# Kernel optimization log

Hardware: AMD Instinct MI355X
Metric: run time of the kernel (lower is better)

The kernel has to match this reference:

```python
import jax, jax.numpy as jnp
import numpy as np

V, H, B = 64, 128, 16384  # num_visible, num_hidden = alpha*V, batch of spin configs
ISCALE = 0.001


def setup_inputs() -> dict:
    key = jax.random.key(0)
    k1, k2, k3, k4 = jax.random.split(key, 4)
    x = jax.random.normal(k1, (B, V), dtype=jnp.float32)
    weight_1 = jax.random.normal(k2, (V, H), dtype=jnp.float32) * ISCALE
    weight_2 = jax.random.normal(k3, (H, V, V), dtype=jnp.float32) * (ISCALE / 10.0)
    hidden_bias = jax.random.normal(k4, (H,), dtype=jnp.float32) * ISCALE
    return {"x": x, "weight_1": weight_1, "weight_2": weight_2, "hidden_bias": hidden_bias}


def reference(x, weight_1, weight_2, hidden_bias):
    b, v = x.shape
    h = weight_2.shape[0]
    # order-1 term: (B,V) @ (V,H) -> (B,H)
    w1 = x @ weight_1
    # order-2 term: outer product of spins per sample, contracted with weight_2.
    # vis_ij: (B,V,V) flattened to (B,V*V); weight_2 flattened to (H,V*V) -> GEMM.
    vis_ij = jnp.einsum('mi,mj->mij', x, x).reshape(b, v * v)
    w2 = (vis_ij @ weight_2.reshape(h, v * v).T) * 0.5
    act = jnp.cos(hidden_bias + w1 + w2)  # (B,H)
    psi = jnp.prod(act, axis=-1)          # (B,)
    return psi
```

## Files before the change

kernel.cpp:

```cpp
#include <hip/hip_runtime.h>
#include <hip/hip_bf16.h>
#include <cstdint>

#define NV 64
#define NH 128
#define NB 16384
#define W2_ELEMS (NH * NV * NV)
#define W1_ELEMS (NV * NH)

typedef __bf16 bf16x8_t __attribute__((ext_vector_type(8)));
typedef float f32x4_t __attribute__((ext_vector_type(4)));
typedef uint32_t u32x4_t __attribute__((ext_vector_type(4)));

__device__ __forceinline__ uint32_t bf16_rne(float f) {
  uint32_t u = __float_as_uint(f);
  return (u + 0x7fffu + ((u >> 16) & 1u)) >> 16;
}

__global__ void cvt_kernel(const float* __restrict__ w1f,
                           const float* __restrict__ w2f,
                           uint16_t* __restrict__ wsW2,
                           uint16_t* __restrict__ wsW1) {
  int base = (blockIdx.x * 256 + threadIdx.x) * 4;
  const float* src;
  uint16_t* dst;
  int off;
  if (base < W2_ELEMS) { src = w2f; dst = wsW2; off = base; }
  else                 { src = w1f; dst = wsW1; off = base - W2_ELEMS; }
  float4 v = *(const float4*)(src + off);
  uint2 p;
  p.x = (bf16_rne(v.y) << 16) | bf16_rne(v.x);
  p.y = (bf16_rne(v.w) << 16) | bf16_rne(v.z);
  *(uint2*)(dst + off) = p;
}

__launch_bounds__(512, 2)
__global__ void rbm_kernel(const float* __restrict__ xg,
                           const float* __restrict__ biasg,
                           const __hip_bfloat16* __restrict__ w1g,
                           const __hip_bfloat16* __restrict__ w2g,
                           float* __restrict__ outg) {
  __shared__ __align__(16) __hip_bfloat16 btile[2][NH * 32];
  __shared__ __align__(16) __hip_bfloat16 xtile[64 * 72];
  __shared__ __align__(16) __hip_bfloat16 w1t[NH * 72];
  __shared__ float part[4][64];

  const int tid  = threadIdx.x;
  const int wv   = tid >> 6;
  const int lane = tid & 63;
  const int c15  = lane & 15;
  const int q    = lane >> 4;
  const int wm   = wv & 1;
  const int hq   = wv >> 1;
  const int mblk = blockIdx.x * 64;

  const int srow = wv * 16 + (lane >> 2);
  const int skg  = lane & 3;
  const int dcg  = skg ^ ((srow >> 1) & 3);
  const size_t gbase = (size_t)srow * 4096 + skg * 8;
  const int dsoff = srow * 32 + dcg * 8;

  uint4 pre = *(const uint4*)(w2g + gbase);

  {
    int row = tid >> 3, grp = tid & 7;
    const float* p = xg + (size_t)(mblk + row) * NV + grp * 8;
    float4 a = *(const float4*)(p);
    float4 b = *(const float4*)(p + 4);
    uint4 o;
    o.x = (bf16_rne(a.y) << 16) | bf16_rne(a.x);
    o.y = (bf16_rne(a.w) << 16) | bf16_rne(a.z);
    o.z = (bf16_rne(b.y) << 16) | bf16_rne(b.x);
    o.w = (bf16_rne(b.w) << 16) | bf16_rne(b.z);
    *(uint4*)(&xtile[row * 72 + grp * 8]) = o;
  }
  {
    int j = tid >> 3, hgrp = tid & 7;
#pragma unroll
    for (int half = 0; half < 2; ++half) {
      int hg = half * 8 + hgrp;
      uint4 v = *(const uint4*)(w1g + (size_t)j * NH + hg * 8);
      const uint32_t d[4] = {v.x, v.y, v.z, v.w};
#pragma unroll
      for (int e = 0; e < 4; ++e) {
        int h0 = hg * 8 + 2 * e;
        ((uint16_t*)w1t)[(h0 + 0) * 72 + j] = (uint16_t)(d[e] & 0xffffu);
        ((uint16_t*)w1t)[(h0 + 1) * 72 + j] = (uint16_t)(d[e] >> 16);
      }
    }
  }
  float xf[2][2][8];
#pragma unroll
  for (int im = 0; im < 2; ++im) {
    int row = mblk + 32 * wm + 16 * im + c15;
#pragma unroll
    for (int jh = 0; jh < 2; ++jh) {
      const float* p = xg + (size_t)row * NV + jh * 32 + q * 8;
      float4 a = *(const float4*)(p);
      float4 b = *(const float4*)(p + 4);
      xf[im][jh][0] = a.x; xf[im][jh][1] = a.y;
      xf[im][jh][2] = a.z; xf[im][jh][3] = a.w;
      xf[im][jh][4] = b.x; xf[im][jh][5] = b.y;
      xf[im][jh][6] = b.z; xf[im][jh][7] = b.w;
    }
  }

  int boff[2];
#pragma unroll
  for (int ih = 0; ih < 2; ++ih) {
    int hrow = 32 * hq + 16 * ih + c15;
    boff[ih] = hrow * 32 + (q ^ ((hrow >> 1) & 3)) * 8;
  }

  f32x4_t acc[2][2];
#pragma unroll
  for (int im = 0; im < 2; ++im)
#pragma unroll
    for (int ih = 0; ih < 2; ++ih)
      acc[im][ih] = (f32x4_t)0.0f;

  float scur[2] = {0.f, 0.f};

#pragma unroll 2
  for (int c = 0; c < 128; ++c) {
    const int buf = c & 1;
    *(uint4*)(&btile[buf][dsoff]) = pre;
    if (c + 1 < 128) pre = *(const uint4*)(w2g + gbase + (size_t)(c + 1) * 32);
    __syncthreads();

    const int jh = c & 1;
    if (jh == 0) {
      int i = c >> 1;
#pragma unroll
      for (int im = 0; im < 2; ++im) {
        int row = 32 * wm + 16 * im + c15;
        uint16_t b = ((const uint16_t*)xtile)[row * 72 + i];
        scur[im] = 0.5f * __uint_as_float(((uint32_t)b) << 16);
      }
    }
    bf16x8_t afrag[2];
#pragma unroll
    for (int im = 0; im < 2; ++im) {
      u32x4_t adv;
#pragma unroll
      for (int t = 0; t < 4; ++t) {
        uint32_t p0 = __float_as_uint(scur[im] * xf[im][jh][2 * t]);
        uint32_t p1 = __float_as_uint(scur[im] * xf[im][jh][2 * t + 1]);
        adv[t] = __builtin_amdgcn_perm(p1, p0, 0x07060302);
      }
      afrag[im] = __builtin_bit_cast(bf16x8_t, adv);
    }
#pragma unroll
    for (int ih = 0; ih < 2; ++ih) {
      bf16x8_t bfrag = *(const bf16x8_t*)(&btile[buf][boff[ih]]);
#pragma unroll
      for (int im = 0; im < 2; ++im)
        acc[im][ih] = __builtin_amdgcn_mfma_f32_16x16x32_bf16(
            afrag[im], bfrag, acc[im][ih], 0, 0, 0);
    }
  }

#pragma unroll
  for (int cc = 0; cc < 2; ++cc) {
    bf16x8_t afrag[2];
#pragma unroll
    for (int im = 0; im < 2; ++im) {
      u32x4_t adv;
#pragma unroll
      for (int t = 0; t < 4; ++t) {
        uint32_t p0 = __float_as_uint(xf[im][cc][2 * t]);
        uint32_t p1 = __float_as_uint(xf[im][cc][2 * t + 1]);
        adv[t] = __builtin_amdgcn_perm(p1, p0, 0x07060302);
      }
      afrag[im] = __builtin_bit_cast(bf16x8_t, adv);
    }
#pragma unroll
    for (int ih = 0; ih < 2; ++ih) {
      int hrow = 32 * hq + 16 * ih + c15;
      bf16x8_t bfrag = *(const bf16x8_t*)(&w1t[hrow * 72 + cc * 32 + q * 8]);
#pragma unroll
      for (int im = 0; im < 2; ++im)
        acc[im][ih] = __builtin_amdgcn_mfma_f32_16x16x32_bf16(
            afrag[im], bfrag, acc[im][ih], 0, 0, 0);
    }
  }

  float bs[2];
#pragma unroll
  for (int ih = 0; ih < 2; ++ih)
    bs[ih] = biasg[32 * hq + 16 * ih + c15];

  float prod[2][4];
#pragma unroll
  for (int im = 0; im < 2; ++im)
#pragma unroll
    for (int r = 0; r < 4; ++r)
      prod[im][r] = cosf(acc[im][0][r] + bs[0]) * cosf(acc[im][1][r] + bs[1]);

#pragma unroll
  for (int ofs = 1; ofs < 16; ofs <<= 1)
#pragma unroll
    for (int im = 0; im < 2; ++im)
#pragma unroll
      for (int r = 0; r < 4; ++r)
        prod[im][r] *= __shfl_xor(prod[im][r], ofs, 16);

  if (c15 == 0) {
#pragma unroll
    for (int im = 0; im < 2; ++im)
#pragma unroll
      for (int r = 0; r < 4; ++r)
        part[hq][32 * wm + 16 * im + 4 * q + r] = prod[im][r];
  }
  __syncthreads();
  if (tid < 64) {
    float f = part[0][tid] * part[1][tid] * part[2][tid] * part[3][tid];
    outg[mblk + tid] = f;
  }
}

extern "C" void kernel_launch(void* const* d_in, const int* in_sizes, int n_in,
                              void* d_out, int out_size, void* d_ws, size_t ws_size,
                              hipStream_t stream) {
  const float* x   = (const float*)d_in[0];
  const float* w1f = (const float*)d_in[1];
  const float* w2f = (const float*)d_in[2];
  const float* hb  = (const float*)d_in[3];
  float* out = (float*)d_out;
  uint16_t* wsW2 = (uint16_t*)d_ws;
  uint16_t* wsW1 = wsW2 + W2_ELEMS;
  (void)in_sizes; (void)n_in; (void)out_size; (void)ws_size;

  cvt_kernel<<<(W2_ELEMS + W1_ELEMS) / (256 * 4), 256, 0, stream>>>(
      w1f, w2f, wsW2, wsW1);
  rbm_kernel<<<NB / 64, 512, 0, stream>>>(
      x, hb, (const __hip_bfloat16*)wsW1, (const __hip_bfloat16*)wsW2, out);
}
```

Measured before the change: 104.8 us.

## Widen W2 chunk to full row per barrier and keep x scale in fp32

The main loop now stages a full 64-wide row of W2 per step, halving the iteration count to 64 and the number of __syncthreads. The next tile is loaded into registers before the MFMAs and stored after them, with a single barrier per step. The 0.5 factor is folded into the W2 conversion, and the x tile is kept as fp32 in LDS, so the scale no longer goes through bf16. W1 is pre-transposed by the conversion kernel and read directly from global memory instead of being staged in LDS, and the per-element products use packed two-wide float multiplies. The trade-off is double the LDS tile size, which may reduce occupancy or pressure registers.

```diff
diff --git a/kernel.cpp b/kernel.cpp
--- a/kernel.cpp
+++ b/kernel.cpp
@@ -10,7 +10,9 @@
 
 typedef __bf16 bf16x8_t __attribute__((ext_vector_type(8)));
 typedef float f32x4_t __attribute__((ext_vector_type(4)));
+typedef float f32x2_t __attribute__((ext_vector_type(2)));
 typedef uint32_t u32x4_t __attribute__((ext_vector_type(4)));
+typedef uint32_t u32x2_t __attribute__((ext_vector_type(2)));
 
 __device__ __forceinline__ uint32_t bf16_rne(float f) {
   uint32_t u = __float_as_uint(f);
@@ -20,29 +22,35 @@
 __global__ void cvt_kernel(const float* __restrict__ w1f,
                            const float* __restrict__ w2f,
                            uint16_t* __restrict__ wsW2,
-                           uint16_t* __restrict__ wsW1) {
+                           uint16_t* __restrict__ wsW1t) {
   int base = (blockIdx.x * 256 + threadIdx.x) * 4;
-  const float* src;
-  uint16_t* dst;
-  int off;
-  if (base < W2_ELEMS) { src = w2f; dst = wsW2; off = base; }
-  else                 { src = w1f; dst = wsW1; off = base - W2_ELEMS; }
-  float4 v = *(const float4*)(src + off);
-  uint2 p;
-  p.x = (bf16_rne(v.y) << 16) | bf16_rne(v.x);
-  p.y = (bf16_rne(v.w) << 16) | bf16_rne(v.z);
-  *(uint2*)(dst + off) = p;
+  if (base < W2_ELEMS) {
+    float4 v = *(const float4*)(w2f + base);
+    uint2 p;
+    p.x = (bf16_rne(0.5f * v.y) << 16) | bf16_rne(0.5f * v.x);
+    p.y = (bf16_rne(0.5f * v.w) << 16) | bf16_rne(0.5f * v.z);
+    *(uint2*)(wsW2 + base) = p;
+  } else {
+    int off = base - W2_ELEMS;
+    float4 v = *(const float4*)(w1f + off);
+    const float d[4] = {v.x, v.y, v.z, v.w};
+#pragma unroll
+    for (int e = 0; e < 4; ++e) {
+      int idx = off + e;
+      int j = idx >> 7, h = idx & 127;
+      wsW1t[h * 64 + j] = (uint16_t)bf16_rne(d[e]);
+    }
+  }
 }
 
 __launch_bounds__(512, 2)
 __global__ void rbm_kernel(const float* __restrict__ xg,
                            const float* __restrict__ biasg,
-                           const __hip_bfloat16* __restrict__ w1g,
+                           const __hip_bfloat16* __restrict__ w1tg,
                            const __hip_bfloat16* __restrict__ w2g,
                            float* __restrict__ outg) {
-  __shared__ __align__(16) __hip_bfloat16 btile[2][NH * 32];
-  __shared__ __align__(16) __hip_bfloat16 xtile[64 * 72];
-  __shared__ __align__(16) __hip_bfloat16 w1t[NH * 72];
+  __shared__ __align__(16) __hip_bfloat16 btile[2][NH * 64];
+  __shared__ __align__(16) float xtile[64 * 68];
   __shared__ float part[4][64];
 
   const int tid  = threadIdx.x;
@@ -54,42 +62,22 @@
   const int hq   = wv >> 1;
   const int mblk = blockIdx.x * 64;
 
-  const int srow = wv * 16 + (lane >> 2);
-  const int skg  = lane & 3;
-  const int dcg  = skg ^ ((srow >> 1) & 3);
-  const size_t gbase = (size_t)srow * 4096 + skg * 8;
-  const int dsoff = srow * 32 + dcg * 8;
-
-  uint4 pre = *(const uint4*)(w2g + gbase);
+  const int sh = tid >> 2;
+  const int g0 = tid & 3, g1 = g0 + 4;
+  const __hip_bfloat16* w2row = w2g + (size_t)sh * 4096;
+  const int d0 = sh * 64 + ((g0 ^ (sh & 7)) * 8);
+  const int d1 = sh * 64 + ((g1 ^ (sh & 7)) * 8);
 
   {
     int row = tid >> 3, grp = tid & 7;
     const float* p = xg + (size_t)(mblk + row) * NV + grp * 8;
     float4 a = *(const float4*)(p);
     float4 b = *(const float4*)(p + 4);
-    uint4 o;
-    o.x = (bf16_rne(a.y) << 16) | bf16_rne(a.x);
-    o.y = (bf16_rne(a.w) << 16) | bf16_rne(a.z);
-    o.z = (bf16_rne(b.y) << 16) | bf16_rne(b.x);
-    o.w = (bf16_rne(b.w) << 16) | bf16_rne(b.z);
-    *(uint4*)(&xtile[row * 72 + grp * 8]) = o;
-  }
-  {
-    int j = tid >> 3, hgrp = tid & 7;
-#pragma unroll
-    for (int half = 0; half < 2; ++half) {
-      int hg = half * 8 + hgrp;
-      uint4 v = *(const uint4*)(w1g + (size_t)j * NH + hg * 8);
-      const uint32_t d[4] = {v.x, v.y, v.z, v.w};
-#pragma unroll
-      for (int e = 0; e < 4; ++e) {
-        int h0 = hg * 8 + 2 * e;
-        ((uint16_t*)w1t)[(h0 + 0) * 72 + j] = (uint16_t)(d[e] & 0xffffu);
-        ((uint16_t*)w1t)[(h0 + 1) * 72 + j] = (uint16_t)(d[e] >> 16);
-      }
-    }
-  }
-  float xf[2][2][8];
+    *(float4*)(&xtile[row * 68 + grp * 8]) = a;
+    *(float4*)(&xtile[row * 68 + grp * 8 + 4]) = b;
+  }
+
+  f32x2_t xf[2][2][4];
 #pragma unroll
   for (int im = 0; im < 2; ++im) {
     int row = mblk + 32 * wm + 16 * im + c15;
@@ -98,19 +86,29 @@
       const float* p = xg + (size_t)row * NV + jh * 32 + q * 8;
       float4 a = *(const float4*)(p);
       float4 b = *(const float4*)(p + 4);
-      xf[im][jh][0] = a.x; xf[im][jh][1] = a.y;
-      xf[im][jh][2] = a.z; xf[im][jh][3] = a.w;
-      xf[im][jh][4] = b.x; xf[im][jh][5] = b.y;
-      xf[im][jh][6] = b.z; xf[im][jh][7] = b.w;
-    }
-  }
-
-  int boff[2];
+      xf[im][jh][0] = f32x2_t{a.x, a.y};
+      xf[im][jh][1] = f32x2_t{a.z, a.w};
+      xf[im][jh][2] = f32x2_t{b.x, b.y};
+      xf[im][jh][3] = f32x2_t{b.z, b.w};
+    }
+  }
+
+  int boff[2][2];
 #pragma unroll
   for (int ih = 0; ih < 2; ++ih) {
     int hrow = 32 * hq + 16 * ih + c15;
-    boff[ih] = hrow * 32 + (q ^ ((hrow >> 1) & 3)) * 8;
-  }
+#pragma unroll
+    for (int jh = 0; jh < 2; ++jh)
+      boff[ih][jh] = hrow * 64 + (((jh * 4 + q) ^ (hrow & 7)) * 8);
+  }
+
+  {
+    uint4 p0 = *(const uint4*)(w2row + g0 * 8);
+    uint4 p1 = *(const uint4*)(w2row + g1 * 8);
+    *(uint4*)(&btile[0][d0]) = p0;
+    *(uint4*)(&btile[0][d1]) = p1;
+  }
+  __syncthreads();
 
   f32x4_t acc[2][2];
 #pragma unroll
@@ -119,65 +117,68 @@
     for (int ih = 0; ih < 2; ++ih)
       acc[im][ih] = (f32x4_t)0.0f;
 
-  float scur[2] = {0.f, 0.f};
-
 #pragma unroll 2
-  for (int c = 0; c < 128; ++c) {
+  for (int c = 0; c < 64; ++c) {
     const int buf = c & 1;
-    *(uint4*)(&btile[buf][dsoff]) = pre;
-    if (c + 1 < 128) pre = *(const uint4*)(w2g + gbase + (size_t)(c + 1) * 32);
-    __syncthreads();
-
-    const int jh = c & 1;
-    if (jh == 0) {
-      int i = c >> 1;
+    uint4 p0, p1;
+    if (c < 63) {
+      const __hip_bfloat16* src = w2row + (c + 1) * 64;
+      p0 = *(const uint4*)(src + g0 * 8);
+      p1 = *(const uint4*)(src + g1 * 8);
+    }
+    float s[2];
+#pragma unroll
+    for (int im = 0; im < 2; ++im)
+      s[im] = xtile[(32 * wm + 16 * im + c15) * 68 + c];
+
+#pragma unroll
+    for (int jh = 0; jh < 2; ++jh) {
+      bf16x8_t afrag[2];
 #pragma unroll
       for (int im = 0; im < 2; ++im) {
-        int row = 32 * wm + 16 * im + c15;
-        uint16_t b = ((const uint16_t*)xtile)[row * 72 + i];
-        scur[im] = 0.5f * __uint_as_float(((uint32_t)b) << 16);
+        const f32x2_t s2 = f32x2_t{s[im], s[im]};
+        u32x4_t adv;
+#pragma unroll
+        for (int t = 0; t < 4; ++t) {
+          f32x2_t pr = s2 * xf[im][jh][t];
+          u32x2_t u = __builtin_bit_cast(u32x2_t, pr);
+          adv[t] = __builtin_amdgcn_perm(u[1], u[0], 0x07060302);
+        }
+        afrag[im] = __builtin_bit_cast(bf16x8_t, adv);
       }
-    }
+#pragma unroll
+      for (int ih = 0; ih < 2; ++ih) {
+        bf16x8_t bfrag = *(const bf16x8_t*)(&btile[buf][boff[ih][jh]]);
+#pragma unroll
+        for (int im = 0; im < 2; ++im)
+          acc[im][ih] = __builtin_amdgcn_mfma_f32_16x16x32_bf16(
+              afrag[im], bfrag, acc[im][ih], 0, 0, 0);
+      }
+    }
+    if (c < 63) {
+      *(uint4*)(&btile[buf ^ 1][d0]) = p0;
+      *(uint4*)(&btile[buf ^ 1][d1]) = p1;
+      __syncthreads();
+    }
+  }
+
+#pragma unroll
+  for (int cc = 0; cc < 2; ++cc) {
     bf16x8_t afrag[2];
 #pragma unroll
     for (int im = 0; im < 2; ++im) {
       u32x4_t adv;
 #pragma unroll
       for (int t = 0; t < 4; ++t) {
-        uint32_t p0 = __float_as_uint(scur[im] * xf[im][jh][2 * t]);
-        uint32_t p1 = __float_as_uint(scur[im] * xf[im][jh][2 * t + 1]);
-        adv[t] = __builtin_amdgcn_perm(p1, p0, 0x07060302);
+        u32x2_t u = __builtin_bit_cast(u32x2_t, xf[im][cc][t]);
+        adv[t] = __builtin_amdgcn_perm(u[1], u[0], 0x07060302);
       }
       afrag[im] = __builtin_bit_cast(bf16x8_t, adv);
     }
 #pragma unroll
     for (int ih = 0; ih < 2; ++ih) {
-      bf16x8_t bfrag = *(const bf16x8_t*)(&btile[buf][boff[ih]]);
-#pragma unroll
-      for (int im = 0; im < 2; ++im)
-        acc[im][ih] = __builtin_amdgcn_mfma_f32_16x16x32_bf16(
-            afrag[im], bfrag, acc[im][ih], 0, 0, 0);
-    }
-  }
-
-#pragma unroll
-  for (int cc = 0; cc < 2; ++cc) {
-    bf16x8_t afrag[2];
-#pragma unroll
-    for (int im = 0; im < 2; ++im) {
-      u32x4_t adv;
-#pragma unroll
-      for (int t = 0; t < 4; ++t) {
-        uint32_t p0 = __float_as_uint(xf[im][cc][2 * t]);
-        uint32_t p1 = __float_as_uint(xf[im][cc][2 * t + 1]);
-        adv[t] = __builtin_amdgcn_perm(p1, p0, 0x07060302);
-      }
-      afrag[im] = __builtin_bit_cast(bf16x8_t, adv);
-    }
-#pragma unroll
-    for (int ih = 0; ih < 2; ++ih) {
       int hrow = 32 * hq + 16 * ih + c15;
-      bf16x8_t bfrag = *(const bf16x8_t*)(&w1t[hrow * 72 + cc * 32 + q * 8]);
+      bf16x8_t bfrag = *(const bf16x8_t*)(w1tg + hrow * 64 + cc * 32 + q * 8);
 #pragma unroll
       for (int im = 0; im < 2; ++im)
         acc[im][ih] = __builtin_amdgcn_mfma_f32_16x16x32_bf16(
@@ -227,12 +228,12 @@
   const float* w2f = (const float*)d_in[2];
   const float* hb  = (const float*)d_in[3];
   float* out = (float*)d_out;
-  uint16_t* wsW2 = (uint16_t*)d_ws;
-  uint16_t* wsW1 = wsW2 + W2_ELEMS;
+  uint16_t* wsW2  = (uint16_t*)d_ws;
+  uint16_t* wsW1t = wsW2 + W2_ELEMS;
   (void)in_sizes; (void)n_in; (void)out_size; (void)ws_size;
 
   cvt_kernel<<<(W2_ELEMS + W1_ELEMS) / (256 * 4), 256, 0, stream>>>(
-      w1f, w2f, wsW2, wsW1);
+      w1f, w2f, wsW2, wsW1t);
   rbm_kernel<<<NB / 64, 512, 0, stream>>>(
-      x, hb, (const __hip_bfloat16*)wsW1, (const __hip_bfloat16*)wsW2, out);
-}
+      x, hb, (const __hip_bfloat16*)wsW1t, (const __hip_bfloat16*)wsW2, out);
+}
```

Result: faster. 99.64 us (-4.9%).
